# Performance work log

Hardware: AMD Instinct MI355X
Metric: run time of the kernel (lower is better)

The kernel has to match this reference:

```python
import jax, jax.numpy as jnp
import numpy as np

N = 8192
IN_F = 512
OUT_F = 64
ALPHA = 0.2  # LeakyReLU negative slope
NEG_INF = -9e15


def setup_inputs() -> dict:
    key = jax.random.key(0)
    k1, k2, k3, k4 = jax.random.split(key, 4)
    x = jax.random.normal(k1, (N, IN_F), dtype=jnp.float32)
    adj = jax.random.randint(k2, (N, N), 0, 2, dtype=jnp.int32)
    # xavier_uniform with gain=1.414
    def xavier(k, shape, gain=1.414):
        fan_in, fan_out = shape[0], shape[1]
        a = gain * np.sqrt(6.0 / (fan_in + fan_out))
        return jax.random.uniform(k, shape, jnp.float32, -a, a)
    W = xavier(k3, (IN_F, OUT_F))
    a = xavier(k4, (2 * OUT_F, 1))
    return {"x": x, "adj": adj, "W": W, "a": a}


def reference(x, adj, W, a):
    h = x @ W  # [N, F]
    f = W.shape[1]
    # e[i,j] = leakyrelu([h_i, h_j] @ a) = leakyrelu(h_i@a1 + h_j@a2)
    e1 = h @ a[:f, 0]   # [N]
    e2 = h @ a[f:, 0]   # [N]
    e = jax.nn.leaky_relu(e1[:, None] + e2[None, :], negative_slope=ALPHA)  # [N, N]
    scores = jnp.where(adj > 0, e, NEG_INF)
    attention = jax.nn.softmax(scores, axis=1)  # dropout p=0.0 -> identity
    h_prime = attention @ h  # [N, F]
    return jax.nn.elu(h_prime)  # concat=True
```

## Files before the change

kernel.cpp:

```cpp
#include <hip/hip_runtime.h>
#include <hip/hip_bf16.h>

#define NN 8192
#define KF 512
#define FF 64
#define GAT_ALPHA 0.2f
#define MSHIFT 20.0f
#define LOG2E 1.44269504f

#define JSPLIT 8
#define JW (NN / JSPLIT)
#define KSTEPS (JW / 32)

#define EXP2F(x) __builtin_amdgcn_exp2f(x)

typedef __attribute__((ext_vector_type(8))) __bf16 bf16x8;
typedef __attribute__((ext_vector_type(4))) float f32x4;
typedef __attribute__((ext_vector_type(4))) int   i32x4;

__device__ __forceinline__ unsigned pack_bf16_rne(float hi, float lo) {
    unsigned uh = __float_as_uint(hi);
    unsigned ul = __float_as_uint(lo);
    uh = uh + 0x7FFFu + ((uh >> 16) & 1u);
    ul = ul + 0x7FFFu + ((ul >> 16) & 1u);
    return (uh & 0xFFFF0000u) | (ul >> 16);
}

__global__ __launch_bounds__(256) void adj_compress(
    const int* __restrict__ adj, unsigned* __restrict__ mask)
{
    const int b   = blockIdx.x * 256 + threadIdx.x;
    const int st4 =  b       & 7;
    const int q   = (b >> 3) & 3;
    const int s   = (b >> 5) & 7;
    const int row =  b >> 8;

    const int* ap = adj + (size_t)row * NN + s * JW + q * 8;
    unsigned w = 0;
    #pragma unroll
    for (int k = 0; k < 4; ++k) {
        const int st = st4 * 4 + k;
        int4 a0 = *(const int4*)(ap + st * 32);
        int4 a1 = *(const int4*)(ap + st * 32 + 4);
        unsigned by =  (unsigned)(a0.x > 0)
                    | ((unsigned)(a0.y > 0) << 1)
                    | ((unsigned)(a0.z > 0) << 2)
                    | ((unsigned)(a0.w > 0) << 3)
                    | ((unsigned)(a1.x > 0) << 4)
                    | ((unsigned)(a1.y > 0) << 5)
                    | ((unsigned)(a1.z > 0) << 6)
                    | ((unsigned)(a1.w > 0) << 7);
        w |= by << (8 * k);
    }
    mask[b] = w;
}

__global__ __launch_bounds__(256) void gat_linear(
    const float* __restrict__ x, const float* __restrict__ W,
    const float* __restrict__ av, __hip_bfloat16* __restrict__ ht,
    float* __restrict__ e1, float* __restrict__ e2)
{
    __shared__ float xs[32][33];
    __shared__ float Ws[32][64];
    __shared__ float ep[2][32][17];

    const int t  = threadIdx.x;
    const int fq = t & 15;
    const int rq = t >> 4;
    const int i0 = blockIdx.x * 32;

    const int kl = t & 31, r0 = t >> 5;
    const int fw = t & 63, kq = t >> 6;

    float acc[2][4] = {};

    for (int kt = 0; kt < KF; kt += 32) {
        #pragma unroll
        for (int m = 0; m < 4; ++m)
            xs[kl][r0 + 8 * m] = x[(size_t)(i0 + r0 + 8 * m) * KF + kt + kl];
        #pragma unroll
        for (int m = 0; m < 8; ++m)
            Ws[kq + 4 * m][fw] = W[(size_t)(kt + kq + 4 * m) * FF + fw];
        __syncthreads();
        #pragma unroll
        for (int kk = 0; kk < 32; ++kk) {
            float x0 = xs[kk][rq * 2];
            float x1 = xs[kk][rq * 2 + 1];
            f32x4 wv = *(const f32x4*)&Ws[kk][fq * 4];
            #pragma unroll
            for (int v = 0; v < 4; ++v) {
                acc[0][v] += x0 * wv[v];
                acc[1][v] += x1 * wv[v];
            }
        }
        __syncthreads();
    }

    #pragma unroll
    for (int v = 0; v < 4; ++v) {
        int f = fq * 4 + v;
        unsigned w = pack_bf16_rne(acc[1][v], acc[0][v]);
        *(unsigned*)&ht[(size_t)f * NN + i0 + rq * 2] = w;
    }

    f32x4 a1v = *(const f32x4*)&av[fq * 4];
    f32x4 a2v = *(const f32x4*)&av[64 + fq * 4];
    #pragma unroll
    for (int u = 0; u < 2; ++u) {
        float s1 = 0.f, s2 = 0.f;
        #pragma unroll
        for (int v = 0; v < 4; ++v) {
            s1 += acc[u][v] * a1v[v];
            s2 += acc[u][v] * a2v[v];
        }
        ep[0][rq * 2 + u][fq] = s1;
        ep[1][rq * 2 + u][fq] = s2;
    }
    __syncthreads();
    if (t < 32) {
        float s1 = 0.f, s2 = 0.f;
        #pragma unroll
        for (int q = 0; q < 16; ++q) { s1 += ep[0][t][q]; s2 += ep[1][t][q]; }
        e1[i0 + t] = s1 * LOG2E;
        e2[i0 + t] = s2 * LOG2E;
    }
}

__global__ __launch_bounds__(256, 4) void gat_attn(
    const unsigned short* __restrict__ maskh, const __hip_bfloat16* __restrict__ ht,
    const float* __restrict__ e1, const float* __restrict__ e2,
    float* __restrict__ accs, float* __restrict__ lsums)
{
    const int t     = threadIdx.x;
    const int lane  = t & 63;
    const int wv    = t >> 6;
    const int n16   = lane & 15;
    const int quad  = lane >> 4;
    const int split = blockIdx.x & (JSPLIT - 1);
    const int i0    = (blockIdx.x >> 3) * 64 + wv * 16;
    const int j0    = split * JW;
    const int row   = i0 + n16;

    const float e1L = e1[row];
    float ms = e1L + MSHIFT * LOG2E;
    const float miL = ms > 0.f ? ms : GAT_ALPHA * ms;
    const float c0  = e1L - miL;
    const float c1  = GAT_ALPHA * e1L - miL;

    const unsigned short* mp  = maskh + (size_t)row * 512 + split * 64 + quad * 16;
    const float*          epx = e2 + j0 + quad * 8;
    const __hip_bfloat16* hp  = ht + (size_t)n16 * NN + j0 + quad * 8;

    f32x4 dacc0 = {0.f,0.f,0.f,0.f}, dacc1 = {0.f,0.f,0.f,0.f};
    f32x4 dacc2 = {0.f,0.f,0.f,0.f}, dacc3 = {0.f,0.f,0.f,0.f};
    f32x4 dl    = {0.f,0.f,0.f,0.f};

    const i32x4 ones_i = {0x3F803F80, 0x3F803F80, 0x3F803F80, 0x3F803F80};
    const bf16x8 ones  = __builtin_bit_cast(bf16x8, ones_i);

    unsigned mh = mp[0];
    for (int c = 0; c < KSTEPS / 2; ++c) {
        const unsigned mcur = mh;
        if (c + 1 < KSTEPS / 2) mh = mp[c + 1];

        #pragma unroll
        for (int k = 0; k < 2; ++k) {
            const int st = c * 2 + k;
            f32x4 e0 = *(const f32x4*)(epx + st * 32);
            f32x4 ev = *(const f32x4*)(epx + st * 32 + 4);
            bf16x8 b0 = *(const bf16x8*)(hp + (size_t)st * 32);
            bf16x8 b1 = *(const bf16x8*)(hp + (size_t)16 * NN + st * 32);
            bf16x8 b2 = *(const bf16x8*)(hp + (size_t)32 * NN + st * 32);
            bf16x8 b3 = *(const bf16x8*)(hp + (size_t)48 * NN + st * 32);

#define PJ(eval, bit)                                                          \
            ( ((mcur >> (bit)) & 1u)                                           \
                ? EXP2F(fmaxf(c0 + (eval), __builtin_fmaf(GAT_ALPHA, (eval), c1))) \
                : 0.f )
            float p0 = PJ(e0.x, k * 8 + 0);
            float p1 = PJ(e0.y, k * 8 + 1);
            float p2 = PJ(e0.z, k * 8 + 2);
            float p3 = PJ(e0.w, k * 8 + 3);
            float p4 = PJ(ev.x, k * 8 + 4);
            float p5 = PJ(ev.y, k * 8 + 5);
            float p6 = PJ(ev.z, k * 8 + 6);
            float p7 = PJ(ev.w, k * 8 + 7);
#undef PJ
            i32x4 iv;
            iv.x = (int)pack_bf16_rne(p1, p0);
            iv.y = (int)pack_bf16_rne(p3, p2);
            iv.z = (int)pack_bf16_rne(p5, p4);
            iv.w = (int)pack_bf16_rne(p7, p6);
            bf16x8 af = __builtin_bit_cast(bf16x8, iv);

            dacc0 = __builtin_amdgcn_mfma_f32_16x16x32_bf16(af, b0, dacc0, 0, 0, 0);
            dacc1 = __builtin_amdgcn_mfma_f32_16x16x32_bf16(af, b1, dacc1, 0, 0, 0);
            dacc2 = __builtin_amdgcn_mfma_f32_16x16x32_bf16(af, b2, dacc2, 0, 0, 0);
            dacc3 = __builtin_amdgcn_mfma_f32_16x16x32_bf16(af, b3, dacc3, 0, 0, 0);
            dl    = __builtin_amdgcn_mfma_f32_16x16x32_bf16(af, ones, dl, 0, 0, 0);
        }
    }

    if (n16 == 0) {
        lsums[(size_t)split * NN + i0 + quad * 4 + 0] = dl.x;
        lsums[(size_t)split * NN + i0 + quad * 4 + 1] = dl.y;
        lsums[(size_t)split * NN + i0 + quad * 4 + 2] = dl.z;
        lsums[(size_t)split * NN + i0 + quad * 4 + 3] = dl.w;
    }

    float* ab = accs + (size_t)split * NN * FF + (size_t)(i0 + quad * 4) * FF + n16;
#define STORE4(dv, ftofs)                                                      \
    ab[0 * FF + (ftofs)] = (dv).x;                                             \
    ab[1 * FF + (ftofs)] = (dv).y;                                             \
    ab[2 * FF + (ftofs)] = (dv).z;                                             \
    ab[3 * FF + (ftofs)] = (dv).w;
    STORE4(dacc0, 0)
    STORE4(dacc1, 16)
    STORE4(dacc2, 32)
    STORE4(dacc3, 48)
#undef STORE4
}

__global__ __launch_bounds__(256) void gat_epilogue(
    const float* __restrict__ accs, const float* __restrict__ lsums,
    float* __restrict__ out)
{
    const int idx = (blockIdx.x * 256 + threadIdx.x) * 4;
    const int row = idx >> 6;

    float l = 0.f;
    #pragma unroll
    for (int s = 0; s < JSPLIT; ++s) l += lsums[(size_t)s * NN + row];

    f32x4 a = {0.f, 0.f, 0.f, 0.f};
    #pragma unroll
    for (int s = 0; s < JSPLIT; ++s) {
        f32x4 v = *(const f32x4*)(accs + (size_t)s * NN * FF + idx);
        a.x += v.x; a.y += v.y; a.z += v.z; a.w += v.w;
    }

    const float li = 1.f / l;
    f32x4 o;
    o.x = a.x * li; o.y = a.y * li; o.z = a.z * li; o.w = a.w * li;
    o.x = o.x > 0.f ? o.x : __expf(o.x) - 1.f;
    o.y = o.y > 0.f ? o.y : __expf(o.y) - 1.f;
    o.z = o.z > 0.f ? o.z : __expf(o.z) - 1.f;
    o.w = o.w > 0.f ? o.w : __expf(o.w) - 1.f;
    *(f32x4*)(out + idx) = o;
}

extern "C" void kernel_launch(void* const* d_in, const int* in_sizes, int n_in,
                              void* d_out, int out_size, void* d_ws, size_t ws_size,
                              hipStream_t stream) {
    const float* x   = (const float*)d_in[0];
    const int*   adj = (const int*)d_in[1];
    const float* W   = (const float*)d_in[2];
    const float* av  = (const float*)d_in[3];
    float* out = (float*)d_out;

    char* wsb = (char*)d_ws;
    __hip_bfloat16* ht = (__hip_bfloat16*)wsb;
    float* e1    = (float*)(wsb + (1 << 20));
    float* e2    = e1 + NN;
    unsigned* mask = (unsigned*)(e2 + NN);
    float* accs  = (float*)((char*)mask + (size_t)NN * 1024);
    float* lsums = accs + (size_t)JSPLIT * NN * FF;

    adj_compress<<<NN * 256 / 256, 256, 0, stream>>>(adj, mask);
    gat_linear<<<256, 256, 0, stream>>>(x, W, av, ht, e1, e2);
    gat_attn<<<(NN / 64) * JSPLIT, 256, 0, stream>>>(
        (const unsigned short*)mask, ht, e1, e2, accs, lsums);
    gat_epilogue<<<NN * FF / 1024, 256, 0, stream>>>(accs, lsums, out);
}
```

Measured before the change: 470.6 us.

## Fuse adjacency compression into attention kernel and stage h/e2 tiles in LDS

Drops the separate adj_compress kernel; each attention block now reads its own 64x512 adjacency tile, packs it to bitmasks in shared memory, and stages its h^T slice and e2 slice in padded LDS. The j-split doubles to 16 and the inner loop becomes a software-pipelined single step that prefetches the next mask byte, e2 values and B fragments from LDS. The aim is to skip the mask write/read round trip and cut global traffic in the hot loop, at the cost of a large LDS footprint (about 76KB per block) limiting occupancy, dropping the launch-bounds occupancy hint, and doubling the partial-accumulator traffic the epilogue must reduce.

```diff
diff --git a/kernel.cpp b/kernel.cpp
--- a/kernel.cpp
+++ b/kernel.cpp
@@ -8,15 +8,16 @@
 #define MSHIFT 20.0f
 #define LOG2E 1.44269504f
 
-#define JSPLIT 8
+#define JSPLIT 16
 #define JW (NN / JSPLIT)
 #define KSTEPS (JW / 32)
 
+#define HTS 520
+
 #define EXP2F(x) __builtin_amdgcn_exp2f(x)
 
 typedef __attribute__((ext_vector_type(8))) __bf16 bf16x8;
 typedef __attribute__((ext_vector_type(4))) float f32x4;
-typedef __attribute__((ext_vector_type(4))) int   i32x4;
 
 __device__ __forceinline__ unsigned pack_bf16_rne(float hi, float lo) {
     unsigned uh = __float_as_uint(hi);
@@ -24,35 +25,6 @@
     uh = uh + 0x7FFFu + ((uh >> 16) & 1u);
     ul = ul + 0x7FFFu + ((ul >> 16) & 1u);
     return (uh & 0xFFFF0000u) | (ul >> 16);
-}
-
-__global__ __launch_bounds__(256) void adj_compress(
-    const int* __restrict__ adj, unsigned* __restrict__ mask)
-{
-    const int b   = blockIdx.x * 256 + threadIdx.x;
-    const int st4 =  b       & 7;
-    const int q   = (b >> 3) & 3;
-    const int s   = (b >> 5) & 7;
-    const int row =  b >> 8;
-
-    const int* ap = adj + (size_t)row * NN + s * JW + q * 8;
-    unsigned w = 0;
-    #pragma unroll
-    for (int k = 0; k < 4; ++k) {
-        const int st = st4 * 4 + k;
-        int4 a0 = *(const int4*)(ap + st * 32);
-        int4 a1 = *(const int4*)(ap + st * 32 + 4);
-        unsigned by =  (unsigned)(a0.x > 0)
-                    | ((unsigned)(a0.y > 0) << 1)
-                    | ((unsigned)(a0.z > 0) << 2)
-                    | ((unsigned)(a0.w > 0) << 3)
-                    | ((unsigned)(a1.x > 0) << 4)
-                    | ((unsigned)(a1.y > 0) << 5)
-                    | ((unsigned)(a1.z > 0) << 6)
-                    | ((unsigned)(a1.w > 0) << 7);
-        w |= by << (8 * k);
-    }
-    mask[b] = w;
 }
 
 __global__ __launch_bounds__(256) void gat_linear(
@@ -126,20 +98,61 @@
     }
 }
 
-__global__ __launch_bounds__(256, 4) void gat_attn(
-    const unsigned short* __restrict__ maskh, const __hip_bfloat16* __restrict__ ht,
+__global__ __launch_bounds__(256) void gat_attn(
+    const int* __restrict__ adj, const __hip_bfloat16* __restrict__ ht,
     const float* __restrict__ e1, const float* __restrict__ e2,
     float* __restrict__ accs, float* __restrict__ lsums)
 {
+    __shared__ __hip_bfloat16 hs[64 * HTS];
+    __shared__ float e2s[JW];
+    __shared__ unsigned char msk[KSTEPS * 4 * 68];
+
     const int t     = threadIdx.x;
     const int lane  = t & 63;
     const int wv    = t >> 6;
     const int n16   = lane & 15;
     const int quad  = lane >> 4;
     const int split = blockIdx.x & (JSPLIT - 1);
-    const int i0    = (blockIdx.x >> 3) * 64 + wv * 16;
+    const int i0b   = (blockIdx.x >> 4) * 64;
+    const int i0    = i0b + wv * 16;
     const int j0    = split * JW;
+    const int rowl  = wv * 16 + n16;
     const int row   = i0 + n16;
+
+    #pragma unroll
+    for (int k = 0; k < 16; ++k) {
+        int g  = t + k * 256;
+        int f  = g >> 6;
+        int jl = (g & 63) * 8;
+        *(bf16x8*)&hs[f * HTS + jl] =
+            *(const bf16x8*)&ht[(size_t)f * NN + j0 + jl];
+    }
+    if (t < JW / 4)
+        *(float4*)&e2s[t * 4] = *(const float4*)&e2[j0 + t * 4];
+
+    {
+        const int st = t & 15;
+        #pragma unroll
+        for (int rep = 0; rep < 4; ++rep) {
+            const int r = rep * 16 + (t >> 4);
+            const int* ap = adj + (size_t)(i0b + r) * NN + j0 + st * 32;
+            unsigned w = 0;
+            #pragma unroll
+            for (int k = 0; k < 8; ++k) {
+                int4 v = *(const int4*)(ap + k * 4);
+                unsigned nib =  (unsigned)(v.x > 0)
+                             | ((unsigned)(v.y > 0) << 1)
+                             | ((unsigned)(v.z > 0) << 2)
+                             | ((unsigned)(v.w > 0) << 3);
+                w |= nib << (k * 4);
+            }
+            msk[(st * 4 + 0) * 68 + r] = (unsigned char)(w       & 0xFF);
+            msk[(st * 4 + 1) * 68 + r] = (unsigned char)((w >> 8)  & 0xFF);
+            msk[(st * 4 + 2) * 68 + r] = (unsigned char)((w >> 16) & 0xFF);
+            msk[(st * 4 + 3) * 68 + r] = (unsigned char)((w >> 24) & 0xFF);
+        }
+    }
+    __syncthreads();
 
     const float e1L = e1[row];
     float ms = e1L + MSHIFT * LOG2E;
@@ -147,58 +160,64 @@
     const float c0  = e1L - miL;
     const float c1  = GAT_ALPHA * e1L - miL;
 
-    const unsigned short* mp  = maskh + (size_t)row * 512 + split * 64 + quad * 16;
-    const float*          epx = e2 + j0 + quad * 8;
-    const __hip_bfloat16* hp  = ht + (size_t)n16 * NN + j0 + quad * 8;
+    const __hip_bfloat16* hp = hs + rowl * 0 + n16 * HTS + quad * 8;
+    const float* ep0 = e2s + quad * 8;
 
     f32x4 dacc0 = {0.f,0.f,0.f,0.f}, dacc1 = {0.f,0.f,0.f,0.f};
     f32x4 dacc2 = {0.f,0.f,0.f,0.f}, dacc3 = {0.f,0.f,0.f,0.f};
     f32x4 dl    = {0.f,0.f,0.f,0.f};
 
+    typedef __attribute__((ext_vector_type(4))) int i32x4;
     const i32x4 ones_i = {0x3F803F80, 0x3F803F80, 0x3F803F80, 0x3F803F80};
     const bf16x8 ones  = __builtin_bit_cast(bf16x8, ones_i);
 
-    unsigned mh = mp[0];
-    for (int c = 0; c < KSTEPS / 2; ++c) {
-        const unsigned mcur = mh;
-        if (c + 1 < KSTEPS / 2) mh = mp[c + 1];
-
-        #pragma unroll
-        for (int k = 0; k < 2; ++k) {
-            const int st = c * 2 + k;
-            f32x4 e0 = *(const f32x4*)(epx + st * 32);
-            f32x4 ev = *(const f32x4*)(epx + st * 32 + 4);
-            bf16x8 b0 = *(const bf16x8*)(hp + (size_t)st * 32);
-            bf16x8 b1 = *(const bf16x8*)(hp + (size_t)16 * NN + st * 32);
-            bf16x8 b2 = *(const bf16x8*)(hp + (size_t)32 * NN + st * 32);
-            bf16x8 b3 = *(const bf16x8*)(hp + (size_t)48 * NN + st * 32);
+    unsigned mb = msk[(0 * 4 + quad) * 68 + rowl];
+    f32x4  e0 = *(const f32x4*)(ep0);
+    f32x4  ev = *(const f32x4*)(ep0 + 4);
+    bf16x8 b0 = *(const bf16x8*)(hp);
+    bf16x8 b1 = *(const bf16x8*)(hp + 16 * HTS);
+    bf16x8 b2 = *(const bf16x8*)(hp + 32 * HTS);
+    bf16x8 b3 = *(const bf16x8*)(hp + 48 * HTS);
+
+    for (int st = 0; st < KSTEPS; ++st) {
+        const unsigned mc = mb;
+        const f32x4  ce0 = e0, cev = ev;
+        const bf16x8 cb0 = b0, cb1 = b1, cb2 = b2, cb3 = b3;
+        if (st + 1 < KSTEPS) {
+            mb = msk[((st + 1) * 4 + quad) * 68 + rowl];
+            e0 = *(const f32x4*)(ep0 + (st + 1) * 32);
+            ev = *(const f32x4*)(ep0 + (st + 1) * 32 + 4);
+            b0 = *(const bf16x8*)(hp + (st + 1) * 32);
+            b1 = *(const bf16x8*)(hp + 16 * HTS + (st + 1) * 32);
+            b2 = *(const bf16x8*)(hp + 32 * HTS + (st + 1) * 32);
+            b3 = *(const bf16x8*)(hp + 48 * HTS + (st + 1) * 32);
+        }
 
 #define PJ(eval, bit)                                                          \
-            ( ((mcur >> (bit)) & 1u)                                           \
-                ? EXP2F(fmaxf(c0 + (eval), __builtin_fmaf(GAT_ALPHA, (eval), c1))) \
-                : 0.f )
-            float p0 = PJ(e0.x, k * 8 + 0);
-            float p1 = PJ(e0.y, k * 8 + 1);
-            float p2 = PJ(e0.z, k * 8 + 2);
-            float p3 = PJ(e0.w, k * 8 + 3);
-            float p4 = PJ(ev.x, k * 8 + 4);
-            float p5 = PJ(ev.y, k * 8 + 5);
-            float p6 = PJ(ev.z, k * 8 + 6);
-            float p7 = PJ(ev.w, k * 8 + 7);
+        ( ((mc >> (bit)) & 1u)                                                 \
+            ? EXP2F(fmaxf(c0 + (eval), __builtin_fmaf(GAT_ALPHA, (eval), c1))) \
+            : 0.f )
+        float p0 = PJ(ce0.x, 0);
+        float p1 = PJ(ce0.y, 1);
+        float p2 = PJ(ce0.z, 2);
+        float p3 = PJ(ce0.w, 3);
+        float p4 = PJ(cev.x, 4);
+        float p5 = PJ(cev.y, 5);
+        float p6 = PJ(cev.z, 6);
+        float p7 = PJ(cev.w, 7);
 #undef PJ
-            i32x4 iv;
-            iv.x = (int)pack_bf16_rne(p1, p0);
-            iv.y = (int)pack_bf16_rne(p3, p2);
-            iv.z = (int)pack_bf16_rne(p5, p4);
-            iv.w = (int)pack_bf16_rne(p7, p6);
-            bf16x8 af = __builtin_bit_cast(bf16x8, iv);
-
-            dacc0 = __builtin_amdgcn_mfma_f32_16x16x32_bf16(af, b0, dacc0, 0, 0, 0);
-            dacc1 = __builtin_amdgcn_mfma_f32_16x16x32_bf16(af, b1, dacc1, 0, 0, 0);
-            dacc2 = __builtin_amdgcn_mfma_f32_16x16x32_bf16(af, b2, dacc2, 0, 0, 0);
-            dacc3 = __builtin_amdgcn_mfma_f32_16x16x32_bf16(af, b3, dacc3, 0, 0, 0);
-            dl    = __builtin_amdgcn_mfma_f32_16x16x32_bf16(af, ones, dl, 0, 0, 0);
-        }
+        i32x4 iv;
+        iv.x = (int)pack_bf16_rne(p1, p0);
+        iv.y = (int)pack_bf16_rne(p3, p2);
+        iv.z = (int)pack_bf16_rne(p5, p4);
+        iv.w = (int)pack_bf16_rne(p7, p6);
+        bf16x8 af = __builtin_bit_cast(bf16x8, iv);
+
+        dacc0 = __builtin_amdgcn_mfma_f32_16x16x32_bf16(af, cb0, dacc0, 0, 0, 0);
+        dacc1 = __builtin_amdgcn_mfma_f32_16x16x32_bf16(af, cb1, dacc1, 0, 0, 0);
+        dacc2 = __builtin_amdgcn_mfma_f32_16x16x32_bf16(af, cb2, dacc2, 0, 0, 0);
+        dacc3 = __builtin_amdgcn_mfma_f32_16x16x32_bf16(af, cb3, dacc3, 0, 0, 0);
+        dl    = __builtin_amdgcn_mfma_f32_16x16x32_bf16(af, ones, dl, 0, 0, 0);
     }
 
     if (n16 == 0) {
@@ -262,13 +281,10 @@
     __hip_bfloat16* ht = (__hip_bfloat16*)wsb;
     float* e1    = (float*)(wsb + (1 << 20));
     float* e2    = e1 + NN;
-    unsigned* mask = (unsigned*)(e2 + NN);
-    float* accs  = (float*)((char*)mask + (size_t)NN * 1024);
+    float* accs  = e2 + NN;
     float* lsums = accs + (size_t)JSPLIT * NN * FF;
 
-    adj_compress<<<NN * 256 / 256, 256, 0, stream>>>(adj, mask);
     gat_linear<<<256, 256, 0, stream>>>(x, W, av, ht, e1, e2);
-    gat_attn<<<(NN / 64) * JSPLIT, 256, 0, stream>>>(
-        (const unsigned short*)mask, ht, e1, e2, accs, lsums);
+    gat_attn<<<(NN / 64) * JSPLIT, 256, 0, stream>>>(adj, ht, e1, e2, accs, lsums);
     gat_epilogue<<<NN * FF / 1024, 256, 0, stream>>>(accs, lsums, out);
 }
```

Measured after the change: 399.8 us. 1.18x faster.
